# Optimization experiments

Hardware: AMD Instinct MI355X
Metric: run time of the kernel (lower is better)

Reference implementation:

```python
import jax, jax.numpy as jnp
import numpy as np

WS = 4            # window_size
C = 192           # dim
NH = 6            # num_heads
HD = C // NH      # head_dim
HID = 384         # mlp hidden = int(dim * mlp_ratio)
EPS = 1e-5


def _rel_pos_index(ws):
    coords = np.stack(np.meshgrid(np.arange(ws), np.arange(ws), np.arange(ws), indexing='ij'))  # [3,ws,ws,ws]
    cf = coords.reshape(3, -1)                                # [3, N]
    rel = cf[:, :, None] - cf[:, None, :]                     # [3, N, N]
    rel = rel.transpose(1, 2, 0)                              # [N, N, 3]
    rel += ws - 1
    rel[:, :, 0] *= (2 * ws - 1) * (2 * ws - 1)
    rel[:, :, 1] *= 2 * ws - 1
    return jnp.asarray(rel.sum(-1), dtype=jnp.int32)          # [N, N]

REL_IDX = _rel_pos_index(WS)


def setup_inputs() -> dict:
    key = jax.random.key(0)
    ks = jax.random.split(key, 20)
    s = 0.02
    B, Dd, Hh, Ww = 2, 48, 48, 48
    L = Dd * Hh * Ww
    tbl = (2 * WS - 1) ** 3
    return {
        'x': jax.random.normal(ks[0], (B, L, C), jnp.float32),
        'D': Dd, 'H': Hh, 'W': Ww,
        'ln1_g': jnp.ones((C,), jnp.float32), 'ln1_b': jnp.zeros((C,), jnp.float32),
        'ln2_g': jnp.ones((C,), jnp.float32), 'ln2_b': jnp.zeros((C,), jnp.float32),
        'qkv_w': jax.random.normal(ks[1], (C, 3 * C), jnp.float32) * s,
        'qkv_b': jnp.zeros((3 * C,), jnp.float32),
        'rpb_table': jax.random.normal(ks[2], (tbl, NH), jnp.float32) * s,
        'proj_w': jax.random.normal(ks[3], (C, C), jnp.float32) * s,
        'proj_b': jnp.zeros((C,), jnp.float32),
        'fc1_w': jax.random.normal(ks[4], (C, HID), jnp.float32) * s,
        'fc1_b': jnp.zeros((HID,), jnp.float32),
        'dw_w': jax.random.normal(ks[5], (HID, 1, 3, 3, 3), jnp.float32) * s,
        'dw_b': jnp.zeros((HID,), jnp.float32),
        'bn_g': jnp.ones((HID,), jnp.float32), 'bn_b': jnp.zeros((HID,), jnp.float32),
        'bn_mean': jnp.zeros((HID,), jnp.float32), 'bn_var': jnp.ones((HID,), jnp.float32),
        'fc2_w': jax.random.normal(ks[6], (HID, C), jnp.float32) * s,
        'fc2_b': jnp.zeros((C,), jnp.float32),
    }


def _ln(x, g, b):
    m = jnp.mean(x, -1, keepdims=True)
    v = jnp.mean((x - m) ** 2, -1, keepdims=True)
    return (x - m) * jax.lax.rsqrt(v + EPS) * g + b


def _window_attn(xw, qkv_w, qkv_b, rpb_table, proj_w, proj_b):
    # xw: [nW, N, C]
    nW, N, _ = xw.shape
    qkv = (xw @ qkv_w + qkv_b).reshape(nW, N, 3, NH, HD)
    q, k, v = qkv[:, :, 0], qkv[:, :, 1], qkv[:, :, 2]   # [nW, N, NH, HD]
    scale = HD ** -0.5
    attn = jnp.einsum('wnhd,wmhd->whnm', q * scale, k)    # [nW, NH, N, N]
    bias = rpb_table[REL_IDX]                              # [N, N, NH]
    attn = attn + jnp.transpose(bias, (2, 0, 1))[None]
    attn = jax.nn.softmax(attn, axis=-1)
    out = jnp.einsum('whnm,wmhd->wnhd', attn, v).reshape(nW, N, C)
    return out @ proj_w + proj_b


def reference(x, D, H, W, ln1_g, ln1_b, ln2_g, ln2_b, qkv_w, qkv_b, rpb_table,
              proj_w, proj_b, fc1_w, fc1_b, dw_w, dw_b, bn_g, bn_b, bn_mean,
              bn_var, fc2_w, fc2_b):
    B, L, _ = x.shape
    shortcut = x
    # --- windowed attention ---
    xs = _ln(x, ln1_g, ln1_b).reshape(B, D, H, W, C)
    # D,H,W divisible by WS -> no padding
    xs = xs.reshape(B, D // WS, WS, H // WS, WS, W // WS, WS, C)
    xw = jnp.transpose(xs, (0, 1, 3, 5, 2, 4, 6, 7)).reshape(-1, WS ** 3, C)
    aw = _window_attn(xw, qkv_w, qkv_b, rpb_table, proj_w, proj_b)
    aw = aw.reshape(B, D // WS, H // WS, W // WS, WS, WS, WS, C)
    xr = jnp.transpose(aw, (0, 1, 4, 2, 5, 3, 6, 7)).reshape(B, L, C)
    x = shortcut + xr
    # --- efficient MLP: fc1 -> dwconv3d -> BN(eval) -> GELU -> fc2 ---
    y = _ln(x, ln2_g, ln2_b)
    h = y @ fc1_w + fc1_b                                  # [B, L, HID]
    hs = jnp.transpose(h, (0, 2, 1)).reshape(B, HID, D, H, W)
    hs = jax.lax.conv_general_dilated(
        hs, dw_w, window_strides=(1, 1, 1), padding='SAME',
        feature_group_count=HID,
        dimension_numbers=('NCDHW', 'OIDHW', 'NCDHW')) + dw_b[None, :, None, None, None]
    hs = (hs - bn_mean[None, :, None, None, None]) * jax.lax.rsqrt(
        bn_var[None, :, None, None, None] + EPS) * bn_g[None, :, None, None, None] + bn_b[None, :, None, None, None]
    h = jnp.transpose(hs.reshape(B, HID, L), (0, 2, 1))
    h = jax.nn.gelu(h, approximate=False)
    return x + (h @ fc2_w + fc2_b)
```

## Files before the change

### kernel.cpp

```cpp
#include <hip/hip_runtime.h>

typedef __bf16 bf16;
typedef __bf16 bf16x8 __attribute__((ext_vector_type(8)));
typedef float f32x4 __attribute__((ext_vector_type(4)));

#define L_TOT 110592
#define TOKS  221184
#define NWIN  3456

static __device__ __forceinline__ f32x4 mfma16(bf16x8 a, bf16x8 b, f32x4 c) {
    return __builtin_amdgcn_mfma_f32_16x16x32_bf16(a, b, c, 0, 0, 0);
}
static __device__ __forceinline__ bf16x8 ld8(const bf16* p) { return *(const bf16x8*)p; }

__global__ void wt_frag(const float* __restrict__ src, bf16* __restrict__ dst, int K, int N) {
    int i = blockIdx.x * 256 + threadIdx.x;
    if (i >= K * N) return;
    int kw = i & 31, col = (i >> 5) & 63, rest = i >> 11;
    int nks = K >> 5;
    int ks = rest % nks, chunk = rest / nks;
    int n = chunk * 64 + col, k = ks * 32 + kw;
    dst[i] = (bf16)src[k * N + n];
}

__global__ void bias6_build(const float* __restrict__ rpb, float* __restrict__ bias6) {
    int i = blockIdx.x * 256 + threadIdx.x;
    if (i >= 6 * 64 * 64) return;
    int h = i >> 12, n = (i >> 6) & 63, m = i & 63;
    int r0 = (n >> 4) - (m >> 4) + 3;
    int r1 = ((n >> 2) & 3) - ((m >> 2) & 3) + 3;
    int r2 = (n & 3) - (m & 3) + 3;
    bias6[i] = rpb[(r0 * 49 + r1 * 7 + r2) * 6 + h];
}

__global__ void ln1_window(const float* __restrict__ x, const float* __restrict__ g,
                           const float* __restrict__ bt, bf16* __restrict__ xw) {
    int wave = threadIdx.x >> 6, lane = threadIdx.x & 63;
    int t = blockIdx.x * 4 + wave;
    const float* row = x + (long)t * 192;
    float v0 = row[lane], v1 = row[lane + 64], v2 = row[lane + 128];
    float s = v0 + v1 + v2;
    #pragma unroll
    for (int m = 1; m < 64; m <<= 1) s += __shfl_xor(s, m);
    float mu = s * (1.0f / 192.0f);
    float d0 = v0 - mu, d1 = v1 - mu, d2 = v2 - mu;
    float q = d0 * d0 + d1 * d1 + d2 * d2;
    #pragma unroll
    for (int m = 1; m < 64; m <<= 1) q += __shfl_xor(q, m);
    float r = rsqrtf(q * (1.0f / 192.0f) + 1e-5f);
    int b = t / L_TOT, l = t - b * L_TOT;
    int dz = l / 2304, rem = l - dz * 2304;
    int hy = rem / 48, wx = rem - hy * 48;
    int w = ((b * 12 + (dz >> 2)) * 12 + (hy >> 2)) * 12 + (wx >> 2);
    int n = (dz & 3) * 16 + (hy & 3) * 4 + (wx & 3);
    bf16* o = xw + (long)w * 12288 + (lane >> 5) * 2048 + n * 32 + (lane & 31);
    o[0]    = (bf16)(d0 * r * g[lane]       + bt[lane]);
    o[4096] = (bf16)(d1 * r * g[lane + 64]  + bt[lane + 64]);
    o[8192] = (bf16)(d2 * r * g[lane + 128] + bt[lane + 128]);
}

__global__ void ln2_kernel(const bf16* __restrict__ in, const float* __restrict__ g,
                           const float* __restrict__ bt, bf16* __restrict__ y) {
    int wave = threadIdx.x >> 6, lane = threadIdx.x & 63;
    long t = blockIdx.x * 4 + wave;
    const bf16* row = in + t * 192;
    float v0 = (float)row[lane], v1 = (float)row[lane + 64], v2 = (float)row[lane + 128];
    float s = v0 + v1 + v2;
    #pragma unroll
    for (int m = 1; m < 64; m <<= 1) s += __shfl_xor(s, m);
    float mu = s * (1.0f / 192.0f);
    float d0 = v0 - mu, d1 = v1 - mu, d2 = v2 - mu;
    float q = d0 * d0 + d1 * d1 + d2 * d2;
    #pragma unroll
    for (int m = 1; m < 64; m <<= 1) q += __shfl_xor(q, m);
    float r = rsqrtf(q * (1.0f / 192.0f) + 1e-5f);
    bf16* o = y + (t >> 6) * 12288 + (lane >> 5) * 2048 + (t & 63) * 32 + (lane & 31);
    o[0]    = (bf16)(d0 * r * g[lane]       + bt[lane]);
    o[4096] = (bf16)(d1 * r * g[lane + 64]  + bt[lane + 64]);
    o[8192] = (bf16)(d2 * r * g[lane + 128] + bt[lane + 128]);
}

__global__ __launch_bounds__(256) void gemm_qkv(
    const bf16* __restrict__ xw, const bf16* __restrict__ wt,
    const float* __restrict__ bqkv,
    bf16* __restrict__ qb, bf16* __restrict__ kb_, bf16* __restrict__ vtb) {
    int m0 = blockIdx.x * 128;
    int w0 = m0 >> 6;
    int wid = threadIdx.x >> 6, lane = threadIdx.x & 63;
    int wr = wid >> 1, wc = wid & 1;
    int lo = lane & 15, hi = lane >> 4;
    f32x4 zf = {0.f, 0.f, 0.f, 0.f};

    const bf16* Ab = xw + (long)(w0 + wr) * 12288 + (lo * 32 + hi * 8);
    bf16x8 a[4][6];
    #pragma unroll
    for (int ti = 0; ti < 4; ++ti)
        #pragma unroll
        for (int ks = 0; ks < 6; ++ks)
            a[ti][ks] = ld8(Ab + ks * 2048 + ti * 512);

    #pragma unroll
    for (int nc = 0; nc < 9; ++nc) {
        int sect = nc / 3;
        int cb0 = (nc - sect * 3) * 64;
        f32x4 acc[4][2];
        #pragma unroll
        for (int i = 0; i < 4; ++i) { acc[i][0] = zf; acc[i][1] = zf; }
        const bf16* Bb = wt + (long)nc * 12288 + (wc * 32 + lo) * 32 + hi * 8;
        #pragma unroll
        for (int ks = 0; ks < 6; ++ks) {
            bf16x8 b0 = ld8(Bb + ks * 2048);
            bf16x8 b1 = ld8(Bb + ks * 2048 + 512);
            #pragma unroll
            for (int ti = 0; ti < 4; ++ti) {
                acc[ti][0] = mfma16(a[ti][ks], b0, acc[ti][0]);
                acc[ti][1] = mfma16(a[ti][ks], b1, acc[ti][1]);
            }
        }
        #pragma unroll
        for (int ti = 0; ti < 4; ++ti)
            #pragma unroll
            for (int j = 0; j < 4; ++j) {
                int trow = m0 + wr * 64 + ti * 16 + hi * 4 + j;
                int w = trow >> 6, n = trow & 63;
                #pragma unroll
                for (int tj = 0; tj < 2; ++tj) {
                    int cw = cb0 + wc * 32 + tj * 16 + lo;
                    int h = cw >> 5, d = cw & 31;
                    float val = acc[ti][tj][j] + bqkv[sect * 192 + cw];
                    long wh = (long)(w * 6 + h);
                    if (sect == 0)       qb[(wh * 64 + n) * 32 + d] = (bf16)(val * 0.17677669529663687f);
                    else if (sect == 1)  kb_[(wh * 64 + n) * 32 + d] = (bf16)val;
                    else                 vtb[(wh * 32 + d) * 64 + n] = (bf16)val;
                }
            }
    }
}

__global__ __launch_bounds__(384) void attn_light(
    const bf16* __restrict__ qb, const bf16* __restrict__ kb_,
    const bf16* __restrict__ vtb, const float* __restrict__ bias6,
    bf16* __restrict__ aw) {
    __shared__ char p_smem[6 * 8192];
    int w = blockIdx.x;
    int h = threadIdx.x >> 6;
    int lane = threadIdx.x & 63;
    int lo = lane & 15, hi = lane >> 4;
    char* ph = p_smem + h * 8192;
    long wh = (long)(w * 6 + h);
    f32x4 zf = {0.f, 0.f, 0.f, 0.f};

    bf16x8 qa[4], kb[4];
    #pragma unroll
    for (int ti = 0; ti < 4; ++ti) qa[ti] = ld8(qb  + (wh * 64 + ti * 16 + lo) * 32 + hi * 8);
    #pragma unroll
    for (int tj = 0; tj < 4; ++tj) kb[tj] = ld8(kb_ + (wh * 64 + tj * 16 + lo) * 32 + hi * 8);
    f32x4 s[4][4];
    #pragma unroll
    for (int ti = 0; ti < 4; ++ti)
        #pragma unroll
        for (int tj = 0; tj < 4; ++tj)
            s[ti][tj] = mfma16(qa[ti], kb[tj], zf);

    const float* bh = bias6 + h * 4096;
    #pragma unroll
    for (int ti = 0; ti < 4; ++ti)
        #pragma unroll
        for (int j = 0; j < 4; ++j) {
            int rr = ti * 16 + hi * 4 + j;
            float ev[4];
            #pragma unroll
            for (int tj = 0; tj < 4; ++tj) s[ti][tj][j] += bh[rr * 64 + tj * 16 + lo];
            float mx = fmaxf(fmaxf(s[ti][0][j], s[ti][1][j]), fmaxf(s[ti][2][j], s[ti][3][j]));
            #pragma unroll
            for (int m = 1; m < 16; m <<= 1) mx = fmaxf(mx, __shfl_xor(mx, m));
            float sum = 0.f;
            #pragma unroll
            for (int tj = 0; tj < 4; ++tj) { ev[tj] = __expf(s[ti][tj][j] - mx); sum += ev[tj]; }
            #pragma unroll
            for (int m = 1; m < 16; m <<= 1) sum += __shfl_xor(sum, m);
            float inv = 1.0f / sum;
            #pragma unroll
            for (int tj = 0; tj < 4; ++tj) {
                int byte = ((rr * 64 + tj * 16 + lo) * 2) ^ ((rr & 7) << 4);
                *(bf16*)(ph + byte) = (bf16)(ev[tj] * inv);
            }
        }

    f32x4 o[4][2];
    #pragma unroll
    for (int i = 0; i < 4; ++i) { o[i][0] = zf; o[i][1] = zf; }
    #pragma unroll
    for (int ks2 = 0; ks2 < 2; ++ks2) {
        bf16x8 pa[4], vb[2];
        #pragma unroll
        for (int ti = 0; ti < 4; ++ti) {
            int row = ti * 16 + lo;
            pa[ti] = *(const bf16x8*)(ph + ((row * 128 + ks2 * 64 + hi * 16) ^ ((row & 7) << 4)));
        }
        #pragma unroll
        for (int td = 0; td < 2; ++td)
            vb[td] = ld8(vtb + (wh * 32 + td * 16 + lo) * 64 + ks2 * 32 + hi * 8);
        #pragma unroll
        for (int ti = 0; ti < 4; ++ti)
            #pragma unroll
            for (int td = 0; td < 2; ++td)
                o[ti][td] = mfma16(pa[ti], vb[td], o[ti][td]);
    }
    bf16* orow = aw + wh * 2048;
    #pragma unroll
    for (int ti = 0; ti < 4; ++ti)
        #pragma unroll
        for (int td = 0; td < 2; ++td)
            #pragma unroll
            for (int j = 0; j < 4; ++j)
                orow[(ti * 16 + hi * 4 + j) * 32 + td * 16 + lo] = (bf16)o[ti][td][j];
}

__global__ __launch_bounds__(256) void gemm_proj(
    const bf16* __restrict__ aw, const bf16* __restrict__ wt,
    const float* __restrict__ bias, const float* __restrict__ x,
    bf16* __restrict__ out1) {
    int m0 = blockIdx.x * 128;
    int w0 = m0 >> 6;
    int wid = threadIdx.x >> 6, lane = threadIdx.x & 63;
    int wr = wid >> 1, wc = wid & 1;
    int lo = lane & 15, hi = lane >> 4;
    f32x4 zf = {0.f, 0.f, 0.f, 0.f};

    const bf16* Ab = aw + (long)(w0 + wr) * 12288 + (lo * 32 + hi * 8);
    bf16x8 a[4][6];
    #pragma unroll
    for (int ti = 0; ti < 4; ++ti)
        #pragma unroll
        for (int ks = 0; ks < 6; ++ks)
            a[ti][ks] = ld8(Ab + ks * 2048 + ti * 512);

    #pragma unroll
    for (int nc = 0; nc < 3; ++nc) {
        f32x4 acc[4][2];
        #pragma unroll
        for (int i = 0; i < 4; ++i) { acc[i][0] = zf; acc[i][1] = zf; }
        const bf16* Bb = wt + (long)nc * 12288 + (wc * 32 + lo) * 32 + hi * 8;
        #pragma unroll
        for (int ks = 0; ks < 6; ++ks) {
            bf16x8 b0 = ld8(Bb + ks * 2048);
            bf16x8 b1 = ld8(Bb + ks * 2048 + 512);
            #pragma unroll
            for (int ti = 0; ti < 4; ++ti) {
                acc[ti][0] = mfma16(a[ti][ks], b0, acc[ti][0]);
                acc[ti][1] = mfma16(a[ti][ks], b1, acc[ti][1]);
            }
        }
        #pragma unroll
        for (int ti = 0; ti < 4; ++ti)
            #pragma unroll
            for (int j = 0; j < 4; ++j) {
                int trow = m0 + wr * 64 + ti * 16 + hi * 4 + j;
                int wv = trow >> 6, n = trow & 63;
                int bb = wv / 1728; int rem = wv - bb * 1728;
                int dq = rem / 144; int rem2 = rem - dq * 144;
                int hq = rem2 / 12; int wq = rem2 - hq * 12;
                int l = (dq * 4 + (n >> 4)) * 2304 + (hq * 4 + ((n >> 2) & 3)) * 48 + (wq * 4 + (n & 3));
                long base = ((long)bb * L_TOT + l) * 192;
                #pragma unroll
                for (int tj = 0; tj < 2; ++tj) {
                    int col = nc * 64 + wc * 32 + tj * 16 + lo;
                    out1[base + col] = (bf16)(x[base + col] + acc[ti][tj][j] + bias[col]);
                }
            }
    }
}

__global__ __launch_bounds__(256) void gemm_fc1(
    const bf16* __restrict__ y, const bf16* __restrict__ wt,
    const float* __restrict__ bias, bf16* __restrict__ h_t) {
    __shared__ bf16 tl[64][136];
    int m0 = blockIdx.x * 128;
    int c0 = m0 >> 6;
    int wid = threadIdx.x >> 6, lane = threadIdx.x & 63;
    int wr = wid >> 1, wc = wid & 1;
    int lo = lane & 15, hi = lane >> 4;
    f32x4 zf = {0.f, 0.f, 0.f, 0.f};
    int bb = m0 / L_TOT; int l0 = m0 - bb * L_TOT;
    int col = threadIdx.x >> 2, seg = threadIdx.x & 3;

    const bf16* Ab = y + (long)(c0 + wr) * 12288 + (lo * 32 + hi * 8);
    bf16x8 a[4][6];
    #pragma unroll
    for (int ti = 0; ti < 4; ++ti)
        #pragma unroll
        for (int ks = 0; ks < 6; ++ks)
            a[ti][ks] = ld8(Ab + ks * 2048 + ti * 512);

    #pragma unroll
    for (int nc = 0; nc < 6; ++nc) {
        f32x4 acc[4][2];
        #pragma unroll
        for (int i = 0; i < 4; ++i) { acc[i][0] = zf; acc[i][1] = zf; }
        const bf16* Bb = wt + (long)nc * 12288 + (wc * 32 + lo) * 32 + hi * 8;
        #pragma unroll
        for (int ks = 0; ks < 6; ++ks) {
            bf16x8 b0 = ld8(Bb + ks * 2048);
            bf16x8 b1 = ld8(Bb + ks * 2048 + 512);
            #pragma unroll
            for (int ti = 0; ti < 4; ++ti) {
                acc[ti][0] = mfma16(a[ti][ks], b0, acc[ti][0]);
                acc[ti][1] = mfma16(a[ti][ks], b1, acc[ti][1]);
            }
        }
        if (nc) __syncthreads();
        #pragma unroll
        for (int ti = 0; ti < 4; ++ti)
            #pragma unroll
            for (int tj = 0; tj < 2; ++tj)
                #pragma unroll
                for (int j = 0; j < 4; ++j) {
                    int rl = wr * 64 + ti * 16 + hi * 4 + j;
                    int cl = wc * 32 + tj * 16 + lo;
                    tl[cl][rl] = (bf16)(acc[ti][tj][j] + bias[nc * 64 + cl]);
                }
        __syncthreads();
        bf16* dst = h_t + ((long)bb * 384 + nc * 64 + col) * L_TOT + l0 + seg * 32;
        #pragma unroll
        for (int i8 = 0; i8 < 4; ++i8)
            *(bf16x8*)(dst + i8 * 8) = *(const bf16x8*)(&tl[col][seg * 32 + i8 * 8]);
    }
}

__global__ __launch_bounds__(320) void dwconv_bn_gelu(
    const bf16* __restrict__ h_t, const float* __restrict__ wconv,
    const float* __restrict__ cb, const float* __restrict__ bng,
    const float* __restrict__ bnb, const float* __restrict__ bnm,
    const float* __restrict__ bnv, bf16* __restrict__ g_t) {
    __shared__ __align__(16) bf16 tile[289 * 56];
    int blk = blockIdx.x;
    int bb = blk / 4608; int rem = blk - bb * 4608;
    int ch = rem / 12; int zb = rem - ch * 12; int z0 = zb * 4;
    const bf16* src = h_t + ((long)bb * 384 + ch) * L_TOT;

    uint4 zv = make_uint4(0u, 0u, 0u, 0u);
    for (int i = threadIdx.x; i < 295; i += 320) {
        int e = (i < 7) ? i * 8 : ((i - 7 + 1) * 56 + 48);
        *(uint4*)(tile + e) = zv;
    }
    for (int c = threadIdx.x; c < 1728; c += 320) {
        int zi = c / 288; int rc = c - zi * 288;
        int r = rc / 6; int cx8 = rc - r * 6;
        int gz = z0 - 1 + zi;
        uint4 val = zv;
        if (gz >= 0 && gz < 48) val = *(const uint4*)(src + (long)gz * 2304 + r * 48 + cx8 * 8);
        *(uint4*)(tile + (1 + zi * 48 + r) * 56 + cx8 * 8) = val;
    }
    float wgt[27];
    #pragma unroll
    for (int i = 0; i < 27; ++i) wgt[i] = wconv[ch * 27 + i];
    float scale = bng[ch] * rsqrtf(bnv[ch] + 1e-5f);
    float shift = bnb[ch] - bnm[ch] * scale;
    float cbias = cb[ch];
    __syncthreads();

    if (threadIdx.x < 288) {
        int y = threadIdx.x / 6, cx = threadIdx.x - y * 6, x0 = cx * 8;
        __builtin_assume(y < 48);
        bool up_ok = (y > 0), dn_ok = (y < 47);
        bf16* dstc = g_t + ((long)bb * 384 + ch) * L_TOT + (long)z0 * 2304 + y * 48 + x0;
        float acc[4][8];
        #pragma unroll
        for (int p = 0; p < 4; ++p)
            #pragma unroll
            for (int k = 0; k < 8; ++k) acc[p][k] = 0.f;

        #pragma unroll
        for (int zi = 0; zi < 6; ++zi) {
            const bf16* plane = tile + (1 + zi * 48) * 56;
            #pragma unroll
            for (int dy = 0; dy < 3; ++dy) {
                bool ok = (dy == 1) || (dy == 0 ? up_ok : dn_ok);
                if (ok) {
                    const bf16* rp = plane + (y + dy - 1) * 56 + x0;
                    bf16x8 mv = ld8(rp);
                    float s[10];
                    s[0] = (float)rp[-1];
                    #pragma unroll
                    for (int i = 0; i < 8; ++i) s[i + 1] = (float)mv[i];
                    s[9] = (float)rp[8];
                    #pragma unroll
                    for (int dz = 0; dz < 3; ++dz) {
                        int p = zi - dz;
                        if (p >= 0 && p <= 3) {
                            float w0 = wgt[dz * 9 + dy * 3 + 0];
                            float w1 = wgt[dz * 9 + dy * 3 + 1];
                            float w2 = wgt[dz * 9 + dy * 3 + 2];
                            #pragma unroll
                            for (int k = 0; k < 8; ++k)
                                acc[p][k] = fmaf(w0, s[k], fmaf(w1, s[k + 1], fmaf(w2, s[k + 2], acc[p][k])));
                        }
                    }
                }
            }
            if (zi >= 2) {
                int p = zi - 2;
                bf16x8 ov;
                #pragma unroll
                for (int k = 0; k < 8; ++k) {
                    float v = acc[p][k] + cbias;
                    v = fmaf(v, scale, shift);
                    float v2 = v * v;
                    float u2 = v * fmaf(v2, 0.0713548162726f, 1.5957691216057308f);
                    float e  = __expf(u2);
                    float q  = __builtin_amdgcn_rcpf(e + 1.0f);
                    ov[k] = (bf16)(v - v * q);
                }
                *(bf16x8*)(dstc + p * 2304) = ov;
            }
        }
    }
}

__global__ __launch_bounds__(256) void gemm_fc2(
    const bf16* __restrict__ g_t, const bf16* __restrict__ wt,
    const float* __restrict__ bias, const bf16* __restrict__ out1,
    float* __restrict__ out) {
    __shared__ bf16 As[2][4096];
    int m0 = blockIdx.x * 64;
    int wc = threadIdx.x >> 6, lane = threadIdx.x & 63;
    int lo = lane & 15, hi = lane >> 4;
    int bb = m0 / L_TOT, l0 = m0 - bb * L_TOT;
    f32x4 zf = {0.f, 0.f, 0.f, 0.f};
    f32x4 acc[3][4];
    #pragma unroll
    for (int tj = 0; tj < 3; ++tj)
        #pragma unroll
        for (int ti = 0; ti < 4; ++ti) acc[tj][ti] = zf;

    int sch = threadIdx.x >> 3;
    int seg = threadIdx.x & 7;
    const bf16* srcb = g_t + ((long)bb * 384 + sch) * L_TOT + l0 + seg * 8;

    bf16x8 r[2];
    #pragma unroll
    for (int p = 0; p < 2; ++p) r[p] = ld8(srcb + (long)(p * 32) * L_TOT);
    #pragma unroll
    for (int p = 0; p < 2; ++p)
        #pragma unroll
        for (int i = 0; i < 8; ++i)
            As[0][(seg * 8 + i) * 64 + ((p * 32 + sch) ^ (((seg ^ i) & 7) << 3))] = r[p][i];

    #pragma unroll
    for (int t = 0; t < 6; ++t) {
        __syncthreads();
        if (t < 5) {
            #pragma unroll
            for (int p = 0; p < 2; ++p)
                r[p] = ld8(srcb + (long)((t + 1) * 64 + p * 32) * L_TOT);
        }
        const bf16* Ac = As[t & 1];
        #pragma unroll
        for (int ksin = 0; ksin < 2; ++ksin) {
            bf16x8 a[4];
            #pragma unroll
            for (int ti = 0; ti < 4; ++ti) {
                int rr = ti * 16 + lo;
                int S = ((rr >> 3) ^ rr) & 7;
                a[ti] = *(const bf16x8*)&Ac[rr * 64 + ((ksin * 32 + hi * 8) ^ (S << 3))];
            }
            #pragma unroll
            for (int tj = 0; tj < 3; ++tj) {
                int cstart = wc * 48 + tj * 16;
                b16_load:;
                bf16x8 b0 = ld8(wt + ((long)((cstart >> 6) * 12 + t * 2 + ksin) * 64 + (cstart & 63) + lo) * 32 + hi * 8);
                #pragma unroll
                for (int ti = 0; ti < 4; ++ti)
                    acc[tj][ti] = mfma16(a[ti], b0, acc[tj][ti]);
            }
        }
        if (t < 5) {
            bf16* An = As[(t + 1) & 1];
            #pragma unroll
            for (int p = 0; p < 2; ++p)
                #pragma unroll
                for (int i = 0; i < 8; ++i)
                    An[(seg * 8 + i) * 64 + ((p * 32 + sch) ^ (((seg ^ i) & 7) << 3))] = r[p][i];
        }
    }
    #pragma unroll
    for (int tj = 0; tj < 3; ++tj)
        #pragma unroll
        for (int ti = 0; ti < 4; ++ti)
            #pragma unroll
            for (int j = 0; j < 4; ++j) {
                long trow = m0 + ti * 16 + hi * 4 + j;
                long base = trow * 192;
                int col = wc * 48 + tj * 16 + lo;
                out[base + col] = (float)out1[base + col] + acc[tj][ti][j] + bias[col];
            }
}

extern "C" void kernel_launch(void* const* d_in, const int* in_sizes, int n_in,
                              void* d_out, int out_size, void* d_ws, size_t ws_size,
                              hipStream_t stream) {
    (void)in_sizes; (void)n_in; (void)out_size; (void)ws_size;
    const float* x     = (const float*)d_in[0];
    const float* ln1g  = (const float*)d_in[4];
    const float* ln1b  = (const float*)d_in[5];
    const float* ln2g  = (const float*)d_in[6];
    const float* ln2b  = (const float*)d_in[7];
    const float* qkvw  = (const float*)d_in[8];
    const float* qkvb  = (const float*)d_in[9];
    const float* rpb   = (const float*)d_in[10];
    const float* projw = (const float*)d_in[11];
    const float* projb = (const float*)d_in[12];
    const float* fc1w  = (const float*)d_in[13];
    const float* fc1b  = (const float*)d_in[14];
    const float* dww   = (const float*)d_in[15];
    const float* dwb   = (const float*)d_in[16];
    const float* bng   = (const float*)d_in[17];
    const float* bnb   = (const float*)d_in[18];
    const float* bnm   = (const float*)d_in[19];
    const float* bnv   = (const float*)d_in[20];
    const float* fc2w  = (const float*)d_in[21];
    const float* fc2b  = (const float*)d_in[22];
    float* out = (float*)d_out;

    char* ws = (char*)d_ws;
    size_t o = 0;
    bf16*  out1 = (bf16*)(ws + o);
    bf16*  vt_buf = (bf16*)(ws + o + 84934656); o += 169869312;
    bf16*  h_t  = (bf16*)(ws + o); o += 169869312;
    bf16*  region1 = (bf16*)(ws + o); o += 169869312;
    bf16*  xw  = region1;
    bf16*  aw  = region1 + 42467328;
    bf16*  yb  = region1;
    bf16*  g_t = region1;
    bf16*  qkvwt  = (bf16*)(ws + o); o += 221184;
    bf16*  projwt = (bf16*)(ws + o); o += 73728;
    bf16*  fc1wt  = (bf16*)(ws + o); o += 147456;
    bf16*  fc2wt  = (bf16*)(ws + o); o += 147456;
    float* bias6  = (float*)(ws + o); o += 98304;

    bf16* q_buf  = h_t;
    bf16* k_buf  = h_t + 42467328;

    wt_frag<<<(110592 + 255) / 256, 256, 0, stream>>>(qkvw, qkvwt, 192, 576);
    wt_frag<<<(36864 + 255) / 256, 256, 0, stream>>>(projw, projwt, 192, 192);
    wt_frag<<<(73728 + 255) / 256, 256, 0, stream>>>(fc1w, fc1wt, 192, 384);
    wt_frag<<<(73728 + 255) / 256, 256, 0, stream>>>(fc2w, fc2wt, 384, 192);
    bias6_build<<<96, 256, 0, stream>>>(rpb, bias6);

    ln1_window<<<55296, 256, 0, stream>>>(x, ln1g, ln1b, xw);
    gemm_qkv<<<1728, 256, 0, stream>>>(xw, qkvwt, qkvb, q_buf, k_buf, vt_buf);
    attn_light<<<NWIN, 384, 0, stream>>>(q_buf, k_buf, vt_buf, bias6, aw);
    gemm_proj<<<1728, 256, 0, stream>>>(aw, projwt, projb, x, out1);
    ln2_kernel<<<55296, 256, 0, stream>>>(out1, ln2g, ln2b, yb);
    gemm_fc1<<<1728, 256, 0, stream>>>(yb, fc1wt, fc1b, h_t);
    dwconv_bn_gelu<<<9216, 320, 0, stream>>>(h_t, dww, dwb, bng, bnb, bnm, bnv, g_t);
    gemm_fc2<<<3456, 256, 0, stream>>>(g_t, fc2wt, fc2b, out1, out);
}
```

Baseline: 756.8 us.

## Use packed FMA in depthwise conv and deepen fc2 prefetch pipeline

The depthwise 3D conv inner loop now works on float2 pairs through packed fma (v_pk_fma_f32), which halves the FMA instruction count at the cost of extra register shuffles to build the even and odd shifted vectors. The fc2 GEMM now prefetches A tiles two stages ahead with a double register buffer, and it loads the residual out1 values into registers before the main loop so their latency overlaps compute. This raises register pressure in both kernels and may lower occupancy.

```diff
diff --git a/kernel.cpp b/kernel.cpp
--- a/kernel.cpp
+++ b/kernel.cpp
@@ -3,6 +3,7 @@
 typedef __bf16 bf16;
 typedef __bf16 bf16x8 __attribute__((ext_vector_type(8)));
 typedef float f32x4 __attribute__((ext_vector_type(4)));
+typedef float f32x2 __attribute__((ext_vector_type(2)));
 
 #define L_TOT 110592
 #define TOKS  221184
@@ -12,6 +13,9 @@
     return __builtin_amdgcn_mfma_f32_16x16x32_bf16(a, b, c, 0, 0, 0);
 }
 static __device__ __forceinline__ bf16x8 ld8(const bf16* p) { return *(const bf16x8*)p; }
+static __device__ __forceinline__ f32x2 pkfma(float w, f32x2 v, f32x2 c) {
+    return __builtin_elementwise_fma((f32x2){w, w}, v, c);
+}
 
 __global__ void wt_frag(const float* __restrict__ src, bf16* __restrict__ dst, int K, int N) {
     int i = blockIdx.x * 256 + threadIdx.x;
@@ -365,11 +369,11 @@
         __builtin_assume(y < 48);
         bool up_ok = (y > 0), dn_ok = (y < 47);
         bf16* dstc = g_t + ((long)bb * 384 + ch) * L_TOT + (long)z0 * 2304 + y * 48 + x0;
-        float acc[4][8];
+        f32x2 accp[4][4];
         #pragma unroll
         for (int p = 0; p < 4; ++p)
             #pragma unroll
-            for (int k = 0; k < 8; ++k) acc[p][k] = 0.f;
+            for (int i = 0; i < 4; ++i) accp[p][i] = (f32x2){0.f, 0.f};
 
         #pragma unroll
         for (int zi = 0; zi < 6; ++zi) {
@@ -380,11 +384,21 @@
                 if (ok) {
                     const bf16* rp = plane + (y + dy - 1) * 56 + x0;
                     bf16x8 mv = ld8(rp);
-                    float s[10];
-                    s[0] = (float)rp[-1];
+                    float d[8];
                     #pragma unroll
-                    for (int i = 0; i < 8; ++i) s[i + 1] = (float)mv[i];
-                    s[9] = (float)rp[8];
+                    for (int i = 0; i < 8; ++i) d[i] = (float)mv[i];
+                    float hl = (float)rp[-1];
+                    float hr = (float)rp[8];
+                    f32x2 E[5], O[4];
+                    E[0] = (f32x2){hl,  d[0]};
+                    E[1] = (f32x2){d[1], d[2]};
+                    E[2] = (f32x2){d[3], d[4]};
+                    E[3] = (f32x2){d[5], d[6]};
+                    E[4] = (f32x2){d[7], hr};
+                    O[0] = (f32x2){d[0], d[1]};
+                    O[1] = (f32x2){d[2], d[3]};
+                    O[2] = (f32x2){d[4], d[5]};
+                    O[3] = (f32x2){d[6], d[7]};
                     #pragma unroll
                     for (int dz = 0; dz < 3; ++dz) {
                         int p = zi - dz;
@@ -393,8 +407,8 @@
                             float w1 = wgt[dz * 9 + dy * 3 + 1];
                             float w2 = wgt[dz * 9 + dy * 3 + 2];
                             #pragma unroll
-                            for (int k = 0; k < 8; ++k)
-                                acc[p][k] = fmaf(w0, s[k], fmaf(w1, s[k + 1], fmaf(w2, s[k + 2], acc[p][k])));
+                            for (int i = 0; i < 4; ++i)
+                                accp[p][i] = pkfma(w0, E[i], pkfma(w1, O[i], pkfma(w2, E[i + 1], accp[p][i])));
                         }
                     }
                 }
@@ -404,7 +418,7 @@
                 bf16x8 ov;
                 #pragma unroll
                 for (int k = 0; k < 8; ++k) {
-                    float v = acc[p][k] + cbias;
+                    float v = accp[p][k >> 1][k & 1] + cbias;
                     v = fmaf(v, scale, shift);
                     float v2 = v * v;
                     float u2 = v * fmaf(v2, 0.0713548162726f, 1.5957691216057308f);
@@ -438,23 +452,33 @@
     int seg = threadIdx.x & 7;
     const bf16* srcb = g_t + ((long)bb * 384 + sch) * L_TOT + l0 + seg * 8;
 
-    bf16x8 r[2];
-    #pragma unroll
-    for (int p = 0; p < 2; ++p) r[p] = ld8(srcb + (long)(p * 32) * L_TOT);
+    bf16x8 r[2][2];
+    #pragma unroll
+    for (int p = 0; p < 2; ++p) r[0][p] = ld8(srcb + (long)(p * 32) * L_TOT);
     #pragma unroll
     for (int p = 0; p < 2; ++p)
         #pragma unroll
         for (int i = 0; i < 8; ++i)
-            As[0][(seg * 8 + i) * 64 + ((p * 32 + sch) ^ (((seg ^ i) & 7) << 3))] = r[p][i];
+            As[0][(seg * 8 + i) * 64 + ((p * 32 + sch) ^ (((seg ^ i) & 7) << 3))] = r[0][p][i];
+    #pragma unroll
+    for (int p = 0; p < 2; ++p) r[0][p] = ld8(srcb + (long)(64 + p * 32) * L_TOT);
+    #pragma unroll
+    for (int p = 0; p < 2; ++p) r[1][p] = ld8(srcb + (long)(128 + p * 32) * L_TOT);
+
+    float res[3][4][4];
+    #pragma unroll
+    for (int tj = 0; tj < 3; ++tj)
+        #pragma unroll
+        for (int ti = 0; ti < 4; ++ti)
+            #pragma unroll
+            for (int j = 0; j < 4; ++j) {
+                long trow = m0 + ti * 16 + hi * 4 + j;
+                res[tj][ti][j] = (float)out1[trow * 192 + wc * 48 + tj * 16 + lo];
+            }
+    __syncthreads();
 
     #pragma unroll
     for (int t = 0; t < 6; ++t) {
-        __syncthreads();
-        if (t < 5) {
-            #pragma unroll
-            for (int p = 0; p < 2; ++p)
-                r[p] = ld8(srcb + (long)((t + 1) * 64 + p * 32) * L_TOT);
-        }
         const bf16* Ac = As[t & 1];
         #pragma unroll
         for (int ksin = 0; ksin < 2; ++ksin) {
@@ -468,7 +492,6 @@
             #pragma unroll
             for (int tj = 0; tj < 3; ++tj) {
                 int cstart = wc * 48 + tj * 16;
-                b16_load:;
                 bf16x8 b0 = ld8(wt + ((long)((cstart >> 6) * 12 + t * 2 + ksin) * 64 + (cstart & 63) + lo) * 32 + hi * 8);
                 #pragma unroll
                 for (int ti = 0; ti < 4; ++ti)
@@ -481,8 +504,14 @@
             for (int p = 0; p < 2; ++p)
                 #pragma unroll
                 for (int i = 0; i < 8; ++i)
-                    An[(seg * 8 + i) * 64 + ((p * 32 + sch) ^ (((seg ^ i) & 7) << 3))] = r[p][i];
-        }
+                    An[(seg * 8 + i) * 64 + ((p * 32 + sch) ^ (((seg ^ i) & 7) << 3))] = r[t & 1][p][i];
+        }
+        if (t < 3) {
+            #pragma unroll
+            for (int p = 0; p < 2; ++p)
+                r[t & 1][p] = ld8(srcb + (long)((t + 3) * 64 + p * 32) * L_TOT);
+        }
+        __syncthreads();
     }
     #pragma unroll
     for (int tj = 0; tj < 3; ++tj)
@@ -491,9 +520,8 @@
             #pragma unroll
             for (int j = 0; j < 4; ++j) {
                 long trow = m0 + ti * 16 + hi * 4 + j;
-                long base = trow * 192;
                 int col = wc * 48 + tj * 16 + lo;
-                out[base + col] = (float)out1[base + col] + acc[tj][ti][j] + bias[col];
+                out[trow * 192 + col] = res[tj][ti][j] + acc[tj][ti][j] + bias[col];
             }
 }
 
```

Result: faster. 739.7 us (-2.3%).
